# Optimization experiments

Hardware: AMD Instinct MI355X
Metric: run time of the kernel (lower is better)

The kernel has to match this reference:

```python
import jax, jax.numpy as jnp
import numpy as np

N_HEAD = 4
GROUPS = 32
EPS = 1e-5


def _group_norm(x, w, b):
    B, C, H, W = x.shape
    g = x.reshape(B, GROUPS, C // GROUPS, H, W)
    mu = g.mean(axis=(2, 3, 4), keepdims=True)
    var = ((g - mu) ** 2).mean(axis=(2, 3, 4), keepdims=True)
    g = (g - mu) * jax.lax.rsqrt(var + EPS)
    return g.reshape(B, C, H, W) * w[None, :, None, None] + b[None, :, None, None]


def _l2norm(x):
    # F.normalize(x, dim=-1): x / max(||x||_2, 1e-12)
    n = jnp.sqrt(jnp.sum(x * x, axis=-1, keepdims=True))
    return x / jnp.maximum(n, 1e-12)


def _masked_softmax(attn, kk):
    # topk indices -> scatter 1s -> masked softmax (faithful to torch scatter_ path)
    idx = jax.lax.top_k(attn, kk)[1]                      # [B,H,c,kk]
    mask = jax.nn.one_hot(idx, attn.shape[-1], dtype=attn.dtype).sum(-2)  # [B,H,c,c]
    return jax.nn.softmax(jnp.where(mask > 0, attn, -jnp.inf), axis=-1)


def setup_inputs() -> dict:
    key = jax.random.key(0)
    ks = jax.random.split(key, 8)
    B, C, H, W = 4, 256, 128, 128
    x = jax.random.normal(ks[0], (B, C, H, W), jnp.float32)
    gn_w = 1.0 + 0.02 * jax.random.normal(ks[1], (C,), jnp.float32)
    gn_b = 0.02 * jax.random.normal(ks[2], (C,), jnp.float32)
    w_qkv = jax.random.normal(ks[3], (3 * C, C), jnp.float32) / np.sqrt(C).astype(np.float32)
    w_dw = jax.random.normal(ks[4], (3 * C, 1, 3, 3), jnp.float32) / 3.0
    w_out = jax.random.normal(ks[5], (C, C), jnp.float32) / np.sqrt(C).astype(np.float32)
    b_out = 0.01 * jax.random.normal(ks[6], (C,), jnp.float32)
    temperature = jnp.ones((N_HEAD, 1, 1), jnp.float32)
    attn_w = jnp.full((4,), 0.2, jnp.float32)  # attn1..attn4 combine weights
    return dict(x=x, gn_w=gn_w, gn_b=gn_b, w_qkv=w_qkv, w_dw=w_dw,
                w_out=w_out, b_out=b_out, temperature=temperature, attn_w=attn_w)


def reference(x, gn_w, gn_b, w_qkv, w_dw, w_out, b_out, temperature, attn_w):
    B, C, H, W = x.shape
    c = C // N_HEAD
    xn = _group_norm(x, gn_w, gn_b)
    # 1x1 conv (no bias)
    qkv = jnp.einsum('oi,bihw->bohw', w_qkv, xn)
    # 3x3 depthwise conv, padding=1, groups=3C, no bias
    qkv = jax.lax.conv_general_dilated(
        qkv, w_dw, window_strides=(1, 1), padding=((1, 1), (1, 1)),
        feature_group_count=3 * C,
        dimension_numbers=('NCHW', 'OIHW', 'NCHW'))
    q, k, v = jnp.split(qkv, 3, axis=1)
    # b (head c) h w -> b head c (h w)
    q = q.reshape(B, N_HEAD, c, H * W)
    k = k.reshape(B, N_HEAD, c, H * W)
    v = v.reshape(B, N_HEAD, c, H * W)
    q = _l2norm(q)
    k = _l2norm(k)
    # FFT cross-correlation attention (fftshift over ALL axes, as torch default)
    q_fft = jnp.fft.fftshift(jnp.fft.rfft2(q))   # [B,H,c,HW//2+1] complex
    k_fft = jnp.fft.fftshift(jnp.fft.rfft2(k))
    attn = jnp.einsum('bhcf,bhdf->bhcd', q_fft, k_fft) * temperature  # complex [B,H,c,c]
    attn = jnp.fft.irfft2(jnp.fft.ifftshift(attn), s=(c, c))          # real [B,H,c,c]
    ks_list = [c // 2, (c * 2) // 3, (c * 3) // 4, (c * 4) // 5]
    out = None
    for i, kk in enumerate(ks_list):
        a = _masked_softmax(attn, kk)
        o = jnp.einsum('bhcd,bhds->bhcs', a, v) * attn_w[i]
        out = o if out is None else out + o
    out = out.reshape(B, C, H, W)
    out = jnp.einsum('oi,bihw->bohw', w_out, out) + b_out[None, :, None, None]
    return out
```

## Files before the change

### kernel.cpp

```cpp
#include <hip/hip_runtime.h>
#include <math.h>

#define NC 256
#define CH3 768
#define HWSZ 16384

typedef __attribute__((ext_vector_type(8))) short short8;
typedef __attribute__((ext_vector_type(4))) float f32x4;
typedef __attribute__((ext_vector_type(4))) unsigned int u32x4;

static const size_t OFF_TW1   = 0;
static const size_t OFF_TW2   = 32768;
static const size_t OFF_HM    = 65536;
static const size_t OFF_SCALE = 65600;
static const size_t OFF_SHIFT = 66624;
static const size_t OFF_PACK  = 67648;
static const size_t OFF_AW    = 182336;
static const size_t OFF_GNP   = 444480;
static const size_t SHARED_END= 446528;

static const size_t R_QKV  = 0;
static const size_t R_SCR  = 12582912;
static const size_t R_H    = 25165824;
static const size_t R_PP   = 29360128;
static const size_t R_RP   = 30408704;
static const size_t R_ATTN = 31457280;
static const size_t R_ACOMB= 31473664;
static const size_t R_PS   = 31490048;
static const size_t R_RS   = 31506432;
static const size_t R_DWP  = 31522816;
static const size_t R_SSUM = 31532032;
static const size_t R_SALT = 31532800;
static const size_t R_SSQ  = 31533568;
static const size_t RSTRIDE= 31534336;

#define TDA_RH 0
#define TDA_RL 8192
#define TDA_IH 16384
#define TDA_IL 24576
#define ETA_RH 32768
#define ETA_RL 40960
#define ETA_IH 49152
#define ETA_IL 57344
#define STB_RH 65536
#define STB_RL 73728
#define STB_IH 81920
#define STB_IL 90112
#define STB_NIH 98304
#define STB_NIL 106496

#define AWQ_H 0
#define AWQ_L 98304
#define AWO_H 196608
#define AWO_L 229376

__device__ inline unsigned short b16rn(float x){
  unsigned u = __float_as_uint(x);
  return (unsigned short)((u + 0x7FFFu + ((u>>16)&1u)) >> 16);
}
__device__ inline unsigned int pk_hi(float x, float y){
  return (__float_as_uint(x)>>16) | (__float_as_uint(y) & 0xFFFF0000u);
}
__device__ inline unsigned int pk_lo(float x, float y){
  float xl = x - __uint_as_float(__float_as_uint(x) & 0xFFFF0000u);
  float yl = y - __uint_as_float(__float_as_uint(y) & 0xFFFF0000u);
  return (unsigned)b16rn(xl) | ((unsigned)b16rn(yl)<<16);
}
__device__ inline short8 ld8g(const unsigned int* p){ return *(const short8*)p; }

__global__ __launch_bounds__(256) void init_tables_k(float* __restrict__ ws){
  int idx = blockIdx.x*256 + threadIdx.x;
  float2* tw1 = (float2*)(ws + OFF_TW1);
  float2* tw2 = (float2*)(ws + OFF_TW2);
  unsigned int* pk = (unsigned int*)(ws + OFF_PACK);
  const double P2 = 6.283185307179586476925286766559005;
  int m = idx >> 7, k = idx & 127;
  double a2 = P2 * (double)(m*k) / 16384.0;
  tw1[idx] = make_float2((float)cos(a2), (float)(-sin(a2)));
  tw2[idx] = make_float2((float)cos(a2), (float)( sin(a2)));
  if (idx < 64){
    double acc = 0.0;
    for (int v = 1; v < 32; v++) acc += sin(P2 * (double)((v*idx) & 63) / 64.0);
    ws[OFF_HM + idx] = (float)(-acc / 32.0);
  }
  if (idx < 8192){
    int r = idx >> 6, kp = idx & 63;
    int k0 = 2*kp, k1 = 2*kp+1;
    double a0 = P2 * (double)((r*k0) & 127) / 128.0;
    double a1 = P2 * (double)((r*k1) & 127) / 128.0;
    float c0 = (float)cos(a0), c1 = (float)cos(a1);
    float s0 = (float)sin(a0), s1 = (float)sin(a1);
    pk[TDA_RH + idx] = pk_hi(c0, c1);  pk[TDA_RL + idx] = pk_lo(c0, c1);
    pk[TDA_IH + idx] = pk_hi(-s0,-s1); pk[TDA_IL + idx] = pk_lo(-s0,-s1);
    pk[ETA_RH + idx] = pk_hi(c0, c1);  pk[ETA_RL + idx] = pk_lo(c0, c1);
    pk[ETA_IH + idx] = pk_hi(s0, s1);  pk[ETA_IL + idx] = pk_lo(s0, s1);
    float sr0, si0, sr1, si1;
    {
      int d0 = (r - k0) & 127, d1 = (r - k1) & 127;
      if (d0 == 0){ sr0 = 64.f; si0 = 0.f; }
      else if ((d0 & 1) == 0){ sr0 = 0.f; si0 = 0.f; }
      else { double th = 3.1415926535897932384626 * (double)d0 / 128.0;
             sr0 = 1.f; si0 = (float)(cos(th)/sin(th)); }
      if (d1 == 0){ sr1 = 64.f; si1 = 0.f; }
      else if ((d1 & 1) == 0){ sr1 = 0.f; si1 = 0.f; }
      else { double th = 3.1415926535897932384626 * (double)d1 / 128.0;
             sr1 = 1.f; si1 = (float)(cos(th)/sin(th)); }
    }
    pk[STB_RH + idx]  = pk_hi(sr0, sr1);  pk[STB_RL + idx]  = pk_lo(sr0, sr1);
    pk[STB_IH + idx]  = pk_hi(si0, si1);  pk[STB_IL + idx]  = pk_lo(si0, si1);
    pk[STB_NIH + idx] = pk_hi(-si0,-si1); pk[STB_NIL + idx] = pk_lo(-si0,-si1);
  }
}

__global__ __launch_bounds__(256) void wpack_k(const float* __restrict__ wqkv, const float* __restrict__ wout,
                                               unsigned int* __restrict__ aw){
  int id = blockIdx.x*256 + threadIdx.x;
  int row = id >> 7, kp = id & 127;
  if (row < CH3){
    float v0 = wqkv[row*256 + 2*kp], v1 = wqkv[row*256 + 2*kp + 1];
    aw[AWQ_H + row*128 + kp] = pk_hi(v0, v1);
    aw[AWQ_L + row*128 + kp] = pk_lo(v0, v1);
  } else {
    int r2 = row - CH3;
    float v0 = wout[r2*256 + 2*kp], v1 = wout[r2*256 + 2*kp + 1];
    aw[AWO_H + r2*128 + kp] = pk_hi(v0, v1);
    aw[AWO_L + r2*128 + kp] = pk_lo(v0, v1);
  }
}

__global__ __launch_bounds__(256) void gn_part_k(const float* __restrict__ x, float2* __restrict__ part){
  int id = blockIdx.x;
  const float4* p = (const float4*)(x + (size_t)id*HWSZ);
  int tid = threadIdx.x;
  float s = 0.f, sq = 0.f;
  #pragma unroll
  for (int i = 0; i < 16; i++){
    float4 v = p[tid + i*256];
    s  += v.x+v.y+v.z+v.w;
    sq += v.x*v.x+v.y*v.y+v.z*v.z+v.w*v.w;
  }
  __shared__ float r1[256], r2[256];
  r1[tid]=s; r2[tid]=sq; __syncthreads();
  for (int off=128; off; off>>=1){
    if (tid<off){ r1[tid]+=r1[tid+off]; r2[tid]+=r2[tid+off]; }
    __syncthreads();
  }
  if (tid==0) part[id] = make_float2(r1[0], r2[0]);
}
__global__ __launch_bounds__(128) void gn_fin_k(const float2* __restrict__ part, const float* __restrict__ gw,
                                                const float* __restrict__ gb, float* __restrict__ scale,
                                                float* __restrict__ shift){
  int bg = threadIdx.x;
  int b = bg >> 5, g = bg & 31;
  float s = 0.f, sq = 0.f;
  #pragma unroll
  for (int i = 0; i < 8; i++){
    float2 v = part[b*NC + g*8 + i];
    s += v.x; sq += v.y;
  }
  const float n = 8.0f*HWSZ;
  float mu = s/n, var = sq/n - mu*mu;
  float rs = rsqrtf(var + 1e-5f);
  for (int i = 0; i < 8; i++){
    int ch = g*8 + i;
    float sc = rs * gw[ch];
    scale[b*NC + ch] = sc;
    shift[b*NC + ch] = gb[ch] - mu*sc;
  }
}

__global__ __launch_bounds__(256) void packx_k(const float* __restrict__ xbase, const float* __restrict__ scale,
                                               const float* __restrict__ shift, float* __restrict__ R0,
                                               size_t rstride){
  int bz = blockIdx.z;
  const float* xb = xbase + (size_t)bz*NC*HWSZ;
  const float* sc = scale + bz*NC;
  const float* sh = shift + bz*NC;
  unsigned int* BqH = (unsigned int*)(R0 + (size_t)bz*rstride + R_H);
  unsigned int* BqL = BqH + 2097152;
  int kb = blockIdx.y;
  int n = blockIdx.x*256 + threadIdx.x;
  float v[8];
  #pragma unroll
  for (int c = 0; c < 8; c++){
    int ch = kb*8 + c;
    v[c] = xb[(size_t)ch*HWSZ + n]*sc[ch] + sh[ch];
  }
  u32x4 h, l;
  #pragma unroll
  for (int q = 0; q < 4; q++){
    h[q] = pk_hi(v[2*q], v[2*q+1]);
    l[q] = pk_lo(v[2*q], v[2*q+1]);
  }
  *(u32x4*)&BqH[((size_t)kb*HWSZ + n)*4] = h;
  *(u32x4*)&BqL[((size_t)kb*HWSZ + n)*4] = l;
}

__global__ __launch_bounds__(256) void gemm_pk(const unsigned int* __restrict__ Ah, const unsigned int* __restrict__ Al,
                                               const unsigned int* __restrict__ Bh0, const unsigned int* __restrict__ Bl0,
                                               const float* __restrict__ bias, float* __restrict__ C0,
                                               size_t bstride, size_t cstride){
  const unsigned int* Bh = Bh0 + (size_t)blockIdx.z*bstride;
  const unsigned int* Bl = Bl0 + (size_t)blockIdx.z*bstride;
  float* C = C0 + (size_t)blockIdx.z*cstride;
  int tid = threadIdx.x;
  int lane = tid & 63, wid = tid >> 6;
  int m0 = blockIdx.y*128, n0 = blockIdx.x*128;
  int wr = (wid>>1)*64, wc = (wid&1)*64;
  int lr = lane & 15, lk = lane >> 4;
  f32x4 acc[4][4] = {};
  size_t aoff[4], boff[4];
  #pragma unroll
  for (int i=0;i<4;i++) aoff[i] = (size_t)(m0 + wr + i*16 + lr)*128 + lk*4;
  #pragma unroll
  for (int j=0;j<4;j++) boff[j] = ((size_t)lk*HWSZ + n0 + wc + j*16 + lr)*4;
  short8 aH[2][4], aL[2][4], bH[2][4], bL[2][4];
  #pragma unroll
  for (int i=0;i<4;i++){ aH[0][i] = ld8g(Ah + aoff[i]); aL[0][i] = ld8g(Al + aoff[i]); }
  #pragma unroll
  for (int j=0;j<4;j++){ bH[0][j] = ld8g(Bh + boff[j]); bL[0][j] = ld8g(Bl + boff[j]); }
  #pragma unroll
  for (int kt = 0; kt < 8; kt++){
    int cur = kt & 1, nxt = cur ^ 1;
    if (kt < 7){
      size_t da = (size_t)(kt+1)*16;
      size_t db = (size_t)(kt+1)*4*HWSZ*4;
      #pragma unroll
      for (int i=0;i<4;i++){ aH[nxt][i] = ld8g(Ah + aoff[i] + da); aL[nxt][i] = ld8g(Al + aoff[i] + da); }
      #pragma unroll
      for (int j=0;j<4;j++){ bH[nxt][j] = ld8g(Bh + boff[j] + db); bL[nxt][j] = ld8g(Bl + boff[j] + db); }
    }
    #pragma unroll
    for (int i=0;i<4;i++)
      #pragma unroll
      for (int j=0;j<4;j++){
        acc[i][j] = __builtin_amdgcn_mfma_f32_16x16x32_bf16(aH[cur][i], bH[cur][j], acc[i][j], 0,0,0);
        acc[i][j] = __builtin_amdgcn_mfma_f32_16x16x32_bf16(aH[cur][i], bL[cur][j], acc[i][j], 0,0,0);
        acc[i][j] = __builtin_amdgcn_mfma_f32_16x16x32_bf16(aL[cur][i], bH[cur][j], acc[i][j], 0,0,0);
      }
  }
  #pragma unroll
  for (int i=0;i<4;i++){
    #pragma unroll
    for (int e=0;e<4;e++){
      int row = m0 + wr + i*16 + lk*4 + e;
      float bb = bias ? bias[row] : 0.0f;
      #pragma unroll
      for (int j=0;j<4;j++)
        C[(size_t)row*HWSZ + n0 + wc + j*16 + lr] = acc[i][j][e] + bb;
    }
  }
}

__global__ __launch_bounds__(256) void dwconv_tiled_k(float* __restrict__ R0, size_t rstride,
                                                      const float* __restrict__ wdw){
  float* Rb = R0 + (size_t)blockIdx.y*rstride;
  int blk = blockIdx.x;
  int ch = blk >> 2, sl = blk & 3;
  int h0 = sl*32;
  const float* in = Rb + R_SCR + (size_t)ch*HWSZ;
  float* outp = Rb + R_QKV + (size_t)ch*HWSZ;
  float* part = Rb + R_DWP;
  float w[9];
  #pragma unroll
  for (int i=0;i<9;i++) w[i] = wdw[ch*9+i];
  __shared__ float tile[34][132];
  __shared__ float r0[256], r1[256], r2[256];
  int tid = threadIdx.x;
  #pragma unroll
  for (int i = 0; i < 5; i++){
    int id = tid + i*256;
    if (id < 1088){
      int r = id >> 5, c4 = id & 31;
      int gh = h0 - 1 + r;
      float4 v = (gh >= 0 && gh < 128) ? *(const float4*)&in[gh*128 + c4*4]
                                       : make_float4(0.f,0.f,0.f,0.f);
      *(float4*)&tile[r][c4*4] = v;
    }
  }
  __syncthreads();
  float s=0.f, sa=0.f, sq=0.f;
  #pragma unroll
  for (int it=0; it<4; it++){
    int idx = it*256 + tid;
    int lh = idx >> 5;
    int xq = idx & 31;
    int xb4 = xq*4;
    float o[4];
    #pragma unroll
    for (int e=0;e<4;e++){
      int xw = xb4 + e;
      float acc = 0.f;
      #pragma unroll
      for (int ky=0; ky<3; ky++){
        const float* tr = &tile[lh+1+ky-1][xw];
        if (xw > 0)   acc += tr[-1]*w[ky*3+0];
                      acc += tr[ 0]*w[ky*3+1];
        if (xw < 127) acc += tr[ 1]*w[ky*3+2];
      }
      o[e] = acc;
      s += acc; sq += acc*acc;
      sa += (e & 1) ? -acc : acc;
    }
    *(float4*)&outp[(h0+lh)*128 + xb4] = make_float4(o[0],o[1],o[2],o[3]);
  }
  r0[tid]=s; r1[tid]=sa; r2[tid]=sq; __syncthreads();
  for (int off=128; off; off>>=1){
    if (tid<off){ r0[tid]+=r0[tid+off]; r1[tid]+=r1[tid+off]; r2[tid]+=r2[tid+off]; }
    __syncthreads();
  }
  if (tid==0){ part[blk]=r0[0]; part[3072+blk]=r1[0]; part[6144+blk]=r2[0]; }
}

__global__ __launch_bounds__(256) void fft1_mfma_k(const float* __restrict__ ws, float* __restrict__ R0,
                                                   size_t rstride){
  float* Rb = R0 + (size_t)blockIdx.y*rstride;
  const float* Kb = Rb + R_QKV + (size_t)256*HWSZ;
  float2* Tc = (float2*)(Rb + R_SCR);
  const unsigned int* PK = (const unsigned int*)(ws + OFF_PACK);
  const float2* tw1 = (const float2*)(ws + OFF_TW1);
  __shared__ unsigned int Bth[128][20], Btl[128][20];
  int tid = threadIdx.x;
  int lane = tid & 63, wid = tid >> 6;
  int wr = (wid>>1)*64, wc = (wid&1)*64;
  int lr = lane & 15, lk = lane >> 4;
  int row = blockIdx.x;
  const float* src = Kb + (size_t)row*HWSZ;
  f32x4 aR[4][4] = {}, aI[4][4] = {};
  int bc = tid & 127, grp = tid >> 7;
  for (int kt = 0; kt < 4; kt++){
    #pragma unroll
    for (int p=0;p<8;p++){
      int kp = grp*8 + p;
      int a = kt*32 + 2*kp;
      float v0 = src[a*128 + bc], v1 = src[(a+1)*128 + bc];
      Bth[bc][kp] = pk_hi(v0, v1);
      Btl[bc][kp] = pk_lo(v0, v1);
    }
    __syncthreads();
    short8 bh[4], bl[4];
    #pragma unroll
    for (int j=0;j<4;j++){
      bh[j] = *(const short8*)&Bth[wc + j*16 + lr][lk*4];
      bl[j] = *(const short8*)&Btl[wc + j*16 + lr][lk*4];
    }
    #pragma unroll
    for (int i=0;i<4;i++){
      int off = (wr + i*16 + lr)*64 + kt*16 + lk*4;
      short8 ahR = ld8g(PK + TDA_RH + off), alR = ld8g(PK + TDA_RL + off);
      short8 ahI = ld8g(PK + TDA_IH + off), alI = ld8g(PK + TDA_IL + off);
      #pragma unroll
      for (int j=0;j<4;j++){
        aR[i][j] = __builtin_amdgcn_mfma_f32_16x16x32_bf16(ahR, bh[j], aR[i][j], 0,0,0);
        aR[i][j] = __builtin_amdgcn_mfma_f32_16x16x32_bf16(ahR, bl[j], aR[i][j], 0,0,0);
        aR[i][j] = __builtin_amdgcn_mfma_f32_16x16x32_bf16(alR, bh[j], aR[i][j], 0,0,0);
        aI[i][j] = __builtin_amdgcn_mfma_f32_16x16x32_bf16(ahI, bh[j], aI[i][j], 0,0,0);
        aI[i][j] = __builtin_amdgcn_mfma_f32_16x16x32_bf16(ahI, bl[j], aI[i][j], 0,0,0);
        aI[i][j] = __builtin_amdgcn_mfma_f32_16x16x32_bf16(alI, bh[j], aI[i][j], 0,0,0);
      }
    }
    __syncthreads();
  }
  #pragma unroll
  for (int i=0;i<4;i++)
    #pragma unroll
    for (int e=0;e<4;e++){
      int m = wr + i*16 + lk*4 + e;
      #pragma unroll
      for (int j=0;j<4;j++){
        int col = wc + j*16 + lr;
        float2 t = tw1[m*128 + col];
        float r = aR[i][j][e], im = aI[i][j][e];
        Tc[(size_t)m*32768 + row*128 + col] = make_float2(r*t.x - im*t.y, r*t.y + im*t.x);
      }
    }
}

__global__ __launch_bounds__(256) void fft2_mfma_k(const float* __restrict__ ws, float* __restrict__ R0,
                                                   size_t rstride){
  float* Rb = R0 + (size_t)blockIdx.y*rstride;
  float2* TU = (float2*)(Rb + R_SCR);
  const unsigned int* PK = (const unsigned int*)(ws + OFF_PACK);
  const float2* tw2 = (const float2*)(ws + OFF_TW2);
  __shared__ unsigned int ARh[128][20], ARl[128][20], AIh[128][20], AIl[128][20];
  int tid = threadIdx.x;
  int lane = tid & 63, wid = tid >> 6;
  int wr = (wid>>1)*64, wc = (wid&1)*64;
  int lr = lane & 15, lk = lane >> 4;
  int m0 = blockIdx.x*128;
  f32x4 aR[4][4] = {}, aI[4][4] = {};
  const float* Tf = (const float*)TU;
  for (int kt = 0; kt < 4; kt++){
    #pragma unroll
    for (int s=0;s<8;s++){
      int id = tid + s*256;
      int r = id >> 4, kp = id & 15;
      int k = kt*32 + 2*kp;
      float4 v = *(const float4*)&Tf[((size_t)(m0+r)*128 + k)*2];
      ARh[r][kp] = pk_hi(v.x, v.z); ARl[r][kp] = pk_lo(v.x, v.z);
      AIh[r][kp] = pk_hi(v.y, v.w); AIl[r][kp] = pk_lo(v.y, v.w);
    }
    __syncthreads();
    short8 ahR[4], alR[4], ahI[4], alI[4];
    #pragma unroll
    for (int i=0;i<4;i++){
      int ar = wr + i*16 + lr;
      ahR[i] = *(const short8*)&ARh[ar][lk*4];
      alR[i] = *(const short8*)&ARl[ar][lk*4];
      ahI[i] = *(const short8*)&AIh[ar][lk*4];
      alI[i] = *(const short8*)&AIl[ar][lk*4];
    }
    #pragma unroll
    for (int j=0;j<4;j++){
      int boff = (wc + j*16 + lr)*64 + kt*16 + lk*4;
      short8 bhR = ld8g(PK + STB_RH + boff), blR = ld8g(PK + STB_RL + boff);
      short8 bhI = ld8g(PK + STB_IH + boff), blI = ld8g(PK + STB_IL + boff);
      short8 bhN = ld8g(PK + STB_NIH + boff), blN = ld8g(PK + STB_NIL + boff);
      #pragma unroll
      for (int i=0;i<4;i++){
        aR[i][j] = __builtin_amdgcn_mfma_f32_16x16x32_bf16(ahR[i], bhR, aR[i][j], 0,0,0);
        aR[i][j] = __builtin_amdgcn_mfma_f32_16x16x32_bf16(ahR[i], blR, aR[i][j], 0,0,0);
        aR[i][j] = __builtin_amdgcn_mfma_f32_16x16x32_bf16(alR[i], bhR, aR[i][j], 0,0,0);
        aR[i][j] = __builtin_amdgcn_mfma_f32_16x16x32_bf16(ahI[i], bhN, aR[i][j], 0,0,0);
        aR[i][j] = __builtin_amdgcn_mfma_f32_16x16x32_bf16(ahI[i], blN, aR[i][j], 0,0,0);
        aR[i][j] = __builtin_amdgcn_mfma_f32_16x16x32_bf16(alI[i], bhN, aR[i][j], 0,0,0);
        aI[i][j] = __builtin_amdgcn_mfma_f32_16x16x32_bf16(ahR[i], bhI, aI[i][j], 0,0,0);
        aI[i][j] = __builtin_amdgcn_mfma_f32_16x16x32_bf16(ahR[i], blI, aI[i][j], 0,0,0);
        aI[i][j] = __builtin_amdgcn_mfma_f32_16x16x32_bf16(alR[i], bhI, aI[i][j], 0,0,0);
        aI[i][j] = __builtin_amdgcn_mfma_f32_16x16x32_bf16(ahI[i], bhR, aI[i][j], 0,0,0);
        aI[i][j] = __builtin_amdgcn_mfma_f32_16x16x32_bf16(ahI[i], blR, aI[i][j], 0,0,0);
        aI[i][j] = __builtin_amdgcn_mfma_f32_16x16x32_bf16(alI[i], bhR, aI[i][j], 0,0,0);
      }
    }
    __syncthreads();
  }
  #pragma unroll
  for (int i=0;i<4;i++)
    #pragma unroll
    for (int e=0;e<4;e++){
      int m = m0 + wr + i*16 + lk*4 + e;
      int f0 = m >> 8;
      #pragma unroll
      for (int j=0;j<4;j++){
        int col = wc + j*16 + lr;
        float2 t = tw2[f0*128 + col];
        float r = aR[i][j][e], im = aI[i][j][e];
        TU[(size_t)m*128 + col] = make_float2(r*t.x - im*t.y, r*t.y + im*t.x);
      }
    }
}

__global__ __launch_bounds__(256) void fft3_mfma_k(const float* __restrict__ ws, float* __restrict__ R0,
                                                   size_t rstride){
  float* Rb = R0 + (size_t)blockIdx.y*rstride;
  const float2* U = (const float2*)(Rb + R_SCR);
  float* Hb = Rb + R_H;
  const unsigned int* PK = (const unsigned int*)(ws + OFF_PACK);
  __shared__ unsigned int BRh[128][20], BRl[128][20], BIh[128][20], BIl[128][20];
  int tid = threadIdx.x;
  int lane = tid & 63, wid = tid >> 6;
  int wr = (wid>>1)*64, wc = (wid&1)*64;
  int lr = lane & 15, lk = lane >> 4;
  int brow = blockIdx.x;
  f32x4 ac[4][4] = {};
  int bc = tid & 127, grp = tid >> 7;
  for (int kt = 0; kt < 4; kt++){
    #pragma unroll
    for (int p=0;p<8;p++){
      int kp = grp*8 + p;
      int k = kt*32 + 2*kp;
      float2 v0 = U[((size_t)k*256 + brow)*128 + bc];
      float2 v1 = U[((size_t)(k+1)*256 + brow)*128 + bc];
      BRh[bc][kp] = pk_hi(v0.x, v1.x); BRl[bc][kp] = pk_lo(v0.x, v1.x);
      BIh[bc][kp] = pk_hi(v0.y, v1.y); BIl[bc][kp] = pk_lo(v0.y, v1.y);
    }
    __syncthreads();
    short8 ahR[4], alR[4], ahI[4], alI[4];
    #pragma unroll
    for (int i=0;i<4;i++){
      int off = (wr + i*16 + lr)*64 + kt*16 + lk*4;
      ahR[i] = ld8g(PK + ETA_RH + off); alR[i] = ld8g(PK + ETA_RL + off);
      ahI[i] = ld8g(PK + ETA_IH + off); alI[i] = ld8g(PK + ETA_IL + off);
    }
    #pragma unroll
    for (int j=0;j<4;j++){
      int col = wc + j*16 + lr;
      short8 bhR = *(const short8*)&BRh[col][lk*4];
      short8 blR = *(const short8*)&BRl[col][lk*4];
      short8 bhI = *(const short8*)&BIh[col][lk*4];
      short8 blI = *(const short8*)&BIl[col][lk*4];
      #pragma unroll
      for (int i=0;i<4;i++){
        ac[i][j] = __builtin_amdgcn_mfma_f32_16x16x32_bf16(ahR[i], bhI, ac[i][j], 0,0,0);
        ac[i][j] = __builtin_amdgcn_mfma_f32_16x16x32_bf16(ahR[i], blI, ac[i][j], 0,0,0);
        ac[i][j] = __builtin_amdgcn_mfma_f32_16x16x32_bf16(alR[i], bhI, ac[i][j], 0,0,0);
        ac[i][j] = __builtin_amdgcn_mfma_f32_16x16x32_bf16(ahI[i], bhR, ac[i][j], 0,0,0);
        ac[i][j] = __builtin_amdgcn_mfma_f32_16x16x32_bf16(ahI[i], blR, ac[i][j], 0,0,0);
        ac[i][j] = __builtin_amdgcn_mfma_f32_16x16x32_bf16(alI[i], bhR, ac[i][j], 0,0,0);
      }
    }
    __syncthreads();
  }
  #pragma unroll
  for (int i=0;i<4;i++)
    #pragma unroll
    for (int e=0;e<4;e++){
      int m = wr + i*16 + lk*4 + e;
      #pragma unroll
      for (int j=0;j<4;j++)
        Hb[(size_t)m*32768 + brow*128 + wc + j*16 + lr] = ac[i][j][e];
    }
}

__global__ __launch_bounds__(256) void pri_k(float* __restrict__ R0, size_t rstride){
  float* Rb = R0 + (size_t)blockIdx.z*rstride;
  const float* qkvdw = Rb + R_QKV;
  const float* Hb = Rb + R_H;
  float* Pp = Rb + R_PP;
  float* Rp = Rb + R_RP;
  int sp = blockIdx.x, head = blockIdx.y;
  const float* Qb = qkvdw + (size_t)(head*64)*HWSZ;
  const float* Kb = qkvdw + (size_t)(256 + head*64)*HWSZ;
  int rowg0 = head*64;
  __shared__ float As[16][65], B1[16][65], B2[16][65];
  int tid=threadIdx.x, tx=tid&15, ty=tid>>4;
  float aP[4][4]={}, aR[4][4]={};
  for (int kc=0;kc<16;kc++){
    int s0 = sp*256 + kc*16;
    #pragma unroll
    for (int i=0;i<4;i++){ int id=tid+i*256; int kk=id&15, m=id>>4;
      As[kk][m] = Qb[(size_t)m*HWSZ + s0+kk]; }
    #pragma unroll
    for (int i=0;i<4;i++){ int id=tid+i*256; int kk=id&15, dd=id>>4;
      int t = (16384 - (s0+kk)) & 16383;
      B1[kk][dd] = Kb[(size_t)dd*HWSZ + t];
      int u = t>>7, r = t&127;
      B2[kk][dd] = Hb[(size_t)u*32768 + (size_t)(rowg0+dd)*128 + r]; }
    __syncthreads();
    #pragma unroll
    for (int k=0;k<16;k++){
      float a[4], b1[4], b2[4];
      #pragma unroll
      for (int i=0;i<4;i++) a[i]=As[k][ty*4+i];
      #pragma unroll
      for (int j=0;j<4;j++){ b1[j]=B1[k][tx*4+j]; b2[j]=B2[k][tx*4+j]; }
      #pragma unroll
      for (int i=0;i<4;i++)
        #pragma unroll
        for (int j=0;j<4;j++){ aP[i][j]+=a[i]*b1[j]; aR[i][j]+=a[i]*b2[j]; }
    }
    __syncthreads();
  }
  size_t base = ((size_t)(sp*4+head))<<12;
  #pragma unroll
  for (int i=0;i<4;i++)
    #pragma unroll
    for (int j=0;j<4;j++){
      size_t o = base + (size_t)(ty*4+i)*64 + tx*4+j;
      Pp[o]=aP[i][j]; Rp[o]=aR[i][j];
    }
}

__global__ __launch_bounds__(256) void red_k(float* __restrict__ R0, size_t rstride){
  float* Rb = R0 + (size_t)blockIdx.y*rstride;
  const float* Pp = Rb + R_PP;
  const float* Rp = Rb + R_RP;
  float* Ps = Rb + R_PS;
  float* Rs = Rb + R_RS;
  int tid = threadIdx.x;
  #pragma unroll
  for (int rep=0; rep<2; rep++){
    int g = blockIdx.x*512 + rep*256 + tid;
    int head = g >> 12, loc = g & 4095;
    float p = 0.f, ri = 0.f;
    for (int sp=0; sp<64; sp++){
      size_t o = ((size_t)(sp*4+head)<<12) + loc;
      p += Pp[o]; ri += Rp[o];
    }
    Ps[g] = p; Rs[g] = ri;
  }
  if (blockIdx.x == 0){
    const float* part = Rb + R_DWP;
    for (int ch = tid; ch < CH3; ch += 256){
      float s=0.f, sa=0.f, sq=0.f;
      #pragma unroll
      for (int sl=0; sl<4; sl++){
        s  += part[ch*4+sl];
        sa += part[3072+ch*4+sl];
        sq += part[6144+ch*4+sl];
      }
      Rb[R_SSUM+ch]=s; Rb[R_SALT+ch]=sa; Rb[R_SSQ+ch]=sq;
    }
  }
}

__global__ __launch_bounds__(256) void attn_build_k(const float* __restrict__ ws, float* __restrict__ R0,
                                                    size_t rstride, const float* __restrict__ temperature){
  float* Rb = R0 + (size_t)blockIdx.y*rstride;
  const float* Ps   = Rb + R_PS;
  const float* Rs   = Rb + R_RS;
  const float* ssum = Rb + R_SSUM;
  const float* salt = Rb + R_SALT;
  const float* ssq  = Rb + R_SSQ;
  float* attn = Rb + R_ATTN;
  const float* hmg  = ws + OFF_HM;
  __shared__ float Rn[64][65], Ril[64][65], hm[64];
  int head = blockIdx.x;
  int tid = threadIdx.x;
  if (tid < 64) hm[tid] = hmg[tid];
  for (int t=0;t<16;t++){
    int idx = tid + t*256; int c = idx>>6, d = idx&63;
    float P = Ps[head*4096 + idx], Ri = Rs[head*4096 + idx];
    int qch = head*64 + c;
    int kch = 256 + head*64 + d;
    float qs=ssum[qch], qa=salt[qch], qn=fmaxf(sqrtf(ssq[qch]), 1e-12f);
    float ks=ssum[kch], ka=salt[kch], kn=fmaxf(sqrtf(ssq[kch]), 1e-12f);
    float Rr = 0.5f*(16384.0f*P + qs*ks + qa*ka);
    float sc = 1.0f/(qn*kn);
    Rn[c][d]  = Rr*sc;
    Ril[c][d] = Ri*sc;
  }
  __syncthreads();
  float tmp2 = temperature[(head+2)&3];
  for (int t=0;t<16;t++){
    int idx = tid + t*256; int c = idx>>6, e = idx&63;
    float s = Rn[c][e];
    #pragma unroll 8
    for (int d=0; d<64; d++) s += Ril[c][d]*hm[(e-d)&63];
    attn[((size_t)head<<12) + (size_t)(c*64+e)] = s*tmp2;
  }
}

__global__ __launch_bounds__(64) void topk_k(float* __restrict__ R0, size_t rstride,
                                             const float* __restrict__ attn_w){
  float* Rb = R0 + (size_t)blockIdx.y*rstride;
  const float* attn = Rb + R_ATTN;
  float* Acomb = Rb + R_ACOMB;
  int blk = blockIdx.x;
  int tid = threadIdx.x;
  __shared__ float row[64];
  float v = attn[(size_t)blk*64 + tid];
  row[tid] = v;
  __syncthreads();
  int rank = 0; float vmax = -1e30f;
  for (int l=0;l<64;l++){
    float w = row[l];
    if (w > v || (w == v && l < tid)) rank++;
    vmax = fmaxf(vmax, w);
  }
  float e = expf(v - vmax);
  const int kks[4] = {32,42,48,51};
  float denom[4];
  #pragma unroll
  for (int i=0;i<4;i++){
    float x = (rank < kks[i]) ? e : 0.0f;
    #pragma unroll
    for (int off=32; off; off>>=1) x += __shfl_xor(x, off);
    denom[i] = x;
  }
  float wgt = 0.f;
  #pragma unroll
  for (int i=0;i<4;i++) if (rank < kks[i]) wgt += attn_w[i] / denom[i];
  Acomb[(size_t)blk*64 + tid] = e * wgt;
}

__global__ __launch_bounds__(256) void av_k(float* __restrict__ R0, size_t rstride){
  float* Rb = R0 + (size_t)blockIdx.z*rstride;
  const float* Acomb = Rb + R_ACOMB;
  unsigned int* BqH = (unsigned int*)(Rb + R_H);
  unsigned int* BqL = BqH + 2097152;
  int head = blockIdx.y;
  int n0 = blockIdx.x*64;
  const float* Vb = Rb + R_QKV + (size_t)(512 + head*64)*HWSZ;
  __shared__ float As[64][65], Bs[16][65];
  int tid=threadIdx.x, tx=tid&15, ty=tid>>4;
  for (int t=0;t<16;t++){ int idx=tid+t*256; As[idx>>6][idx&63] = Acomb[((size_t)head<<12)+idx]; }
  __syncthreads();
  float acc[4][4]={};
  for (int k0=0;k0<64;k0+=16){
    #pragma unroll
    for (int i=0;i<4;i++){ int id=tid+i*256; int nn=id&63, k=id>>6;
      Bs[k][nn] = Vb[(size_t)(k0+k)*HWSZ + n0+nn]; }
    __syncthreads();
    #pragma unroll
    for (int k=0;k<16;k++){
      float a[4], bv[4];
      #pragma unroll
      for (int i=0;i<4;i++) a[i]=As[ty*4+i][k0+k];
      #pragma unroll
      for (int j=0;j<4;j++) bv[j]=Bs[k][tx*4+j];
      #pragma unroll
      for (int i=0;i<4;i++)
        #pragma unroll
        for (int j=0;j<4;j++) acc[i][j] += a[i]*bv[j];
    }
    __syncthreads();
  }
  int kpa = head*32 + ty*2;
  int kba = kpa >> 2, qa = kpa & 3;
  int kpb = kpa + 1;
  int kbb = kpb >> 2, qb = kpb & 3;
  #pragma unroll
  for (int j=0;j<4;j++){
    int n = n0 + tx*4 + j;
    BqH[((size_t)kba*HWSZ + n)*4 + qa] = pk_hi(acc[0][j], acc[1][j]);
    BqL[((size_t)kba*HWSZ + n)*4 + qa] = pk_lo(acc[0][j], acc[1][j]);
    BqH[((size_t)kbb*HWSZ + n)*4 + qb] = pk_hi(acc[2][j], acc[3][j]);
    BqL[((size_t)kbb*HWSZ + n)*4 + qb] = pk_lo(acc[2][j], acc[3][j]);
  }
}

extern "C" void kernel_launch(void* const* d_in, const int* in_sizes, int n_in,
                              void* d_out, int out_size, void* d_ws, size_t ws_size,
                              hipStream_t stream) {
  const float* x     = (const float*)d_in[0];
  const float* gn_w  = (const float*)d_in[1];
  const float* gn_b  = (const float*)d_in[2];
  const float* w_qkv = (const float*)d_in[3];
  const float* w_dw  = (const float*)d_in[4];
  const float* w_out = (const float*)d_in[5];
  const float* b_out = (const float*)d_in[6];
  const float* temperature = (const float*)d_in[7];
  const float* attn_w = (const float*)d_in[8];
  float* out = (float*)d_out;
  float* ws  = (float*)d_ws;
  unsigned int* AW = (unsigned int*)(ws + OFF_AW);
  float* R0 = ws + SHARED_END;
  const size_t CHW = (size_t)NC*HWSZ;

  size_t need2 = (SHARED_END + 2*RSTRIDE)*sizeof(float);
  size_t need4 = (SHARED_END + 4*RSTRIDE)*sizeof(float);
  int zb = (ws_size >= need4) ? 4 : (ws_size >= need2) ? 2 : 1;

  init_tables_k<<<64,256,0,stream>>>(ws);
  wpack_k<<<512,256,0,stream>>>(w_qkv, w_out, AW);
  gn_part_k<<<1024,256,0,stream>>>(x, (float2*)(ws+OFF_GNP));
  gn_fin_k<<<1,128,0,stream>>>((const float2*)(ws+OFF_GNP), gn_w, gn_b,
                               ws+OFF_SCALE, ws+OFF_SHIFT);

  for (int b0 = 0; b0 < 4; b0 += zb){
    packx_k<<<dim3(64,32,zb),256,0,stream>>>(x + (size_t)b0*CHW, ws+OFF_SCALE+b0*NC,
                                             ws+OFF_SHIFT+b0*NC, R0, RSTRIDE);
    gemm_pk<<<dim3(128,6,zb),256,0,stream>>>(AW+AWQ_H, AW+AWQ_L,
                                             (unsigned int*)(R0+R_H), (unsigned int*)(R0+R_H)+2097152,
                                             nullptr, R0+R_SCR, RSTRIDE, RSTRIDE);
    dwconv_tiled_k<<<dim3(3072,zb),256,0,stream>>>(R0, RSTRIDE, w_dw);
    fft1_mfma_k<<<dim3(256,zb),256,0,stream>>>(ws, R0, RSTRIDE);
    fft2_mfma_k<<<dim3(256,zb),256,0,stream>>>(ws, R0, RSTRIDE);
    fft3_mfma_k<<<dim3(256,zb),256,0,stream>>>(ws, R0, RSTRIDE);
    pri_k<<<dim3(64,4,zb),256,0,stream>>>(R0, RSTRIDE);
    red_k<<<dim3(32,zb),256,0,stream>>>(R0, RSTRIDE);
    attn_build_k<<<dim3(4,zb),256,0,stream>>>(ws, R0, RSTRIDE, temperature);
    topk_k<<<dim3(256,zb),64,0,stream>>>(R0, RSTRIDE, attn_w);
    av_k<<<dim3(256,4,zb),256,0,stream>>>(R0, RSTRIDE);
    gemm_pk<<<dim3(128,2,zb),256,0,stream>>>(AW+AWO_H, AW+AWO_L,
                                             (unsigned int*)(R0+R_H), (unsigned int*)(R0+R_H)+2097152,
                                             b_out, out + (size_t)b0*CHW, RSTRIDE, CHW);
  }
}
```

Before: 859.1 us.

## Move pri correlation to split-bf16 MFMA and pre-reverse fft3 output layout

Rewrites the pri kernel from scalar FP32 FMA tiles to split-bf16 (hi/lo) MFMA, with operands packed into LDS. fft3 now writes its output already index-reversed and laid out per row, so pri reads it contiguously instead of through a strided gather. The projection GEMM also moves from double to triple register buffering of global loads, which raises register pressure. The split-bf16 trick drops the lo*lo term, so the correlation loses a little precision compared with full FP32.

Measured after the change: 828.4 us. -3.6%, faster.

```diff
diff --git a/kernel.cpp b/kernel.cpp
--- a/kernel.cpp
+++ b/kernel.cpp
@@ -214,22 +214,19 @@
   for (int i=0;i<4;i++) aoff[i] = (size_t)(m0 + wr + i*16 + lr)*128 + lk*4;
   #pragma unroll
   for (int j=0;j<4;j++) boff[j] = ((size_t)lk*HWSZ + n0 + wc + j*16 + lr)*4;
-  short8 aH[2][4], aL[2][4], bH[2][4], bL[2][4];
-  #pragma unroll
-  for (int i=0;i<4;i++){ aH[0][i] = ld8g(Ah + aoff[i]); aL[0][i] = ld8g(Al + aoff[i]); }
-  #pragma unroll
-  for (int j=0;j<4;j++){ bH[0][j] = ld8g(Bh + boff[j]); bL[0][j] = ld8g(Bl + boff[j]); }
+  short8 aH[3][4], aL[3][4], bH[3][4], bL[3][4];
+#define LOADT(B,T) { \
+    size_t da = (size_t)(T)*16, db = (size_t)(T)*4*HWSZ*4; \
+    _Pragma("unroll") \
+    for (int i=0;i<4;i++){ aH[B][i] = ld8g(Ah + aoff[i] + da); aL[B][i] = ld8g(Al + aoff[i] + da); } \
+    _Pragma("unroll") \
+    for (int j=0;j<4;j++){ bH[B][j] = ld8g(Bh + boff[j] + db); bL[B][j] = ld8g(Bl + boff[j] + db); } \
+  }
+  LOADT(0,0); LOADT(1,1);
   #pragma unroll
   for (int kt = 0; kt < 8; kt++){
-    int cur = kt & 1, nxt = cur ^ 1;
-    if (kt < 7){
-      size_t da = (size_t)(kt+1)*16;
-      size_t db = (size_t)(kt+1)*4*HWSZ*4;
-      #pragma unroll
-      for (int i=0;i<4;i++){ aH[nxt][i] = ld8g(Ah + aoff[i] + da); aL[nxt][i] = ld8g(Al + aoff[i] + da); }
-      #pragma unroll
-      for (int j=0;j<4;j++){ bH[nxt][j] = ld8g(Bh + boff[j] + db); bL[nxt][j] = ld8g(Bl + boff[j] + db); }
-    }
+    int cur = kt % 3;
+    if (kt < 6){ int nb = (kt+2) % 3; LOADT(nb, kt+2); }
     #pragma unroll
     for (int i=0;i<4;i++)
       #pragma unroll
@@ -239,6 +236,7 @@
         acc[i][j] = __builtin_amdgcn_mfma_f32_16x16x32_bf16(aL[cur][i], bH[cur][j], acc[i][j], 0,0,0);
       }
   }
+#undef LOADT
   #pragma unroll
   for (int i=0;i<4;i++){
     #pragma unroll
@@ -293,7 +291,7 @@
       float acc = 0.f;
       #pragma unroll
       for (int ky=0; ky<3; ky++){
-        const float* tr = &tile[lh+1+ky-1][xw];
+        const float* tr = &tile[lh+ky][xw];
         if (xw > 0)   acc += tr[-1]*w[ky*3+0];
                       acc += tr[ 0]*w[ky*3+1];
         if (xw < 127) acc += tr[ 1]*w[ky*3+2];
@@ -454,7 +452,7 @@
                                                    size_t rstride){
   float* Rb = R0 + (size_t)blockIdx.y*rstride;
   const float2* U = (const float2*)(Rb + R_SCR);
-  float* Hb = Rb + R_H;
+  float* Hf = Rb + R_H;
   const unsigned int* PK = (const unsigned int*)(ws + OFF_PACK);
   __shared__ unsigned int BRh[128][20], BRl[128][20], BIh[128][20], BIl[128][20];
   int tid = threadIdx.x;
@@ -507,57 +505,82 @@
     for (int e=0;e<4;e++){
       int m = wr + i*16 + lk*4 + e;
       #pragma unroll
-      for (int j=0;j<4;j++)
-        Hb[(size_t)m*32768 + brow*128 + wc + j*16 + lr] = ac[i][j][e];
-    }
-}
-
-__global__ __launch_bounds__(256) void pri_k(float* __restrict__ R0, size_t rstride){
+      for (int j=0;j<4;j++){
+        int col = wc + j*16 + lr;
+        int s = (16384 - (m*128 + col)) & 16383;
+        Hf[(size_t)brow*16384 + s] = ac[i][j][e];
+      }
+    }
+}
+
+__global__ __launch_bounds__(256) void pri2_k(float* __restrict__ R0, size_t rstride){
   float* Rb = R0 + (size_t)blockIdx.z*rstride;
-  const float* qkvdw = Rb + R_QKV;
-  const float* Hb = Rb + R_H;
+  int sp = blockIdx.x, head = blockIdx.y;
+  const float* Qb = Rb + R_QKV + (size_t)(head*64)*HWSZ;
+  const float* Kb = Rb + R_QKV + (size_t)(256 + head*64)*HWSZ;
+  const float* Hf = Rb + R_H + (size_t)(head*64)*16384;
   float* Pp = Rb + R_PP;
   float* Rp = Rb + R_RP;
-  int sp = blockIdx.x, head = blockIdx.y;
-  const float* Qb = qkvdw + (size_t)(head*64)*HWSZ;
-  const float* Kb = qkvdw + (size_t)(256 + head*64)*HWSZ;
-  int rowg0 = head*64;
-  __shared__ float As[16][65], B1[16][65], B2[16][65];
-  int tid=threadIdx.x, tx=tid&15, ty=tid>>4;
-  float aP[4][4]={}, aR[4][4]={};
-  for (int kc=0;kc<16;kc++){
-    int s0 = sp*256 + kc*16;
-    #pragma unroll
-    for (int i=0;i<4;i++){ int id=tid+i*256; int kk=id&15, m=id>>4;
-      As[kk][m] = Qb[(size_t)m*HWSZ + s0+kk]; }
-    #pragma unroll
-    for (int i=0;i<4;i++){ int id=tid+i*256; int kk=id&15, dd=id>>4;
-      int t = (16384 - (s0+kk)) & 16383;
-      B1[kk][dd] = Kb[(size_t)dd*HWSZ + t];
-      int u = t>>7, r = t&127;
-      B2[kk][dd] = Hb[(size_t)u*32768 + (size_t)(rowg0+dd)*128 + r]; }
-    __syncthreads();
-    #pragma unroll
-    for (int k=0;k<16;k++){
-      float a[4], b1[4], b2[4];
-      #pragma unroll
-      for (int i=0;i<4;i++) a[i]=As[k][ty*4+i];
-      #pragma unroll
-      for (int j=0;j<4;j++){ b1[j]=B1[k][tx*4+j]; b2[j]=B2[k][tx*4+j]; }
-      #pragma unroll
-      for (int i=0;i<4;i++)
-        #pragma unroll
-        for (int j=0;j<4;j++){ aP[i][j]+=a[i]*b1[j]; aR[i][j]+=a[i]*b2[j]; }
-    }
-    __syncthreads();
-  }
-  size_t base = ((size_t)(sp*4+head))<<12;
-  #pragma unroll
-  for (int i=0;i<4;i++)
-    #pragma unroll
-    for (int j=0;j<4;j++){
-      size_t o = base + (size_t)(ty*4+i)*64 + tx*4+j;
-      Pp[o]=aP[i][j]; Rp[o]=aR[i][j];
+  __shared__ unsigned int Qh[64][17], Ql[64][17], K1h[64][17], K1l[64][17], K2h[64][17], K2l[64][17];
+  int tid = threadIdx.x, lane = tid & 63, wid = tid >> 6;
+  int wr = (wid>>1)*32, wc = (wid&1)*32;
+  int lr = lane & 15, lk = lane >> 4;
+  int sd = tid >> 2, sk0 = (tid & 3)*8;
+  f32x4 aP[2][2] = {}, aR[2][2] = {};
+  for (int kt = 0; kt < 8; kt++){
+    int s0 = sp*256 + kt*32;
+    float q[8], k1[8], k2[8];
+    #pragma unroll
+    for (int e=0;e<8;e++){
+      int s = s0 + sk0 + e;
+      q[e]  = Qb[(size_t)sd*HWSZ + s];
+      k1[e] = Kb[(size_t)sd*HWSZ + ((16384 - s) & 16383)];
+      k2[e] = Hf[(size_t)sd*16384 + s];
+    }
+    __syncthreads();
+    #pragma unroll
+    for (int p=0;p<4;p++){
+      int kp = (sk0>>1) + p;
+      Qh[sd][kp]  = pk_hi(q[2*p],  q[2*p+1]);  Ql[sd][kp]  = pk_lo(q[2*p],  q[2*p+1]);
+      K1h[sd][kp] = pk_hi(k1[2*p], k1[2*p+1]); K1l[sd][kp] = pk_lo(k1[2*p], k1[2*p+1]);
+      K2h[sd][kp] = pk_hi(k2[2*p], k2[2*p+1]); K2l[sd][kp] = pk_lo(k2[2*p], k2[2*p+1]);
+    }
+    __syncthreads();
+    short8 qh[2], ql[2], b1h[2], b1l[2], b2h[2], b2l[2];
+    #pragma unroll
+    for (int i=0;i<2;i++){
+      qh[i]  = *(const short8*)&Qh[wr + i*16 + lr][lk*4];
+      ql[i]  = *(const short8*)&Ql[wr + i*16 + lr][lk*4];
+      b1h[i] = *(const short8*)&K1h[wc + i*16 + lr][lk*4];
+      b1l[i] = *(const short8*)&K1l[wc + i*16 + lr][lk*4];
+      b2h[i] = *(const short8*)&K2h[wc + i*16 + lr][lk*4];
+      b2l[i] = *(const short8*)&K2l[wc + i*16 + lr][lk*4];
+    }
+    #pragma unroll
+    for (int i=0;i<2;i++)
+      #pragma unroll
+      for (int j=0;j<2;j++){
+        aP[i][j] = __builtin_amdgcn_mfma_f32_16x16x32_bf16(qh[i], b1h[j], aP[i][j], 0,0,0);
+        aP[i][j] = __builtin_amdgcn_mfma_f32_16x16x32_bf16(qh[i], b1l[j], aP[i][j], 0,0,0);
+        aP[i][j] = __builtin_amdgcn_mfma_f32_16x16x32_bf16(ql[i], b1h[j], aP[i][j], 0,0,0);
+        aR[i][j] = __builtin_amdgcn_mfma_f32_16x16x32_bf16(qh[i], b2h[j], aR[i][j], 0,0,0);
+        aR[i][j] = __builtin_amdgcn_mfma_f32_16x16x32_bf16(qh[i], b2l[j], aR[i][j], 0,0,0);
+        aR[i][j] = __builtin_amdgcn_mfma_f32_16x16x32_bf16(ql[i], b2h[j], aR[i][j], 0,0,0);
+      }
+  }
+  size_t base = ((size_t)(sp*4 + head)) << 12;
+  #pragma unroll
+  for (int i=0;i<2;i++)
+    #pragma unroll
+    for (int e=0;e<4;e++){
+      int row = wr + i*16 + lk*4 + e;
+      #pragma unroll
+      for (int j=0;j<2;j++){
+        int col = wc + j*16 + lr;
+        size_t o = base + (size_t)row*64 + col;
+        Pp[o] = aP[i][j][e];
+        Rp[o] = aR[i][j][e];
+      }
     }
 }
 
@@ -748,7 +771,7 @@
     fft1_mfma_k<<<dim3(256,zb),256,0,stream>>>(ws, R0, RSTRIDE);
     fft2_mfma_k<<<dim3(256,zb),256,0,stream>>>(ws, R0, RSTRIDE);
     fft3_mfma_k<<<dim3(256,zb),256,0,stream>>>(ws, R0, RSTRIDE);
-    pri_k<<<dim3(64,4,zb),256,0,stream>>>(R0, RSTRIDE);
+    pri2_k<<<dim3(64,4,zb),256,0,stream>>>(R0, RSTRIDE);
     red_k<<<dim3(32,zb),256,0,stream>>>(R0, RSTRIDE);
     attn_build_k<<<dim3(4,zb),256,0,stream>>>(ws, R0, RSTRIDE, temperature);
     topk_k<<<dim3(256,zb),64,0,stream>>>(R0, RSTRIDE, attn_w);
```

## Rewrite pri kernel with split-bf16 MFMA and pre-reversed bf16 operand layouts

Applied to the files above, without the earlier changes.

The fp32 scalar-FMA pri_k GEMM is replaced by pri3_k, which uses bf16x3-style split-precision MFMA instructions. The dwconv kernel now also emits Q as hi/lo bf16 pairs with the spatial index reversed, and K as hi/lo bf16 pairs. fft3 writes its output in a transposed hi/lo bf16 layout so pri3 can do contiguous vector loads instead of gathered strided loads. The aim is to remove the scalar FMA and gather cost, at the price of extra writes in dwconv and fft3 and reduced precision from the split-bf16 approximation.

Result: faster. 825.1 us (-4.0%).

```diff
diff --git a/kernel.cpp b/kernel.cpp
--- a/kernel.cpp
+++ b/kernel.cpp
@@ -33,6 +33,7 @@
 static const size_t R_SALT = 31532800;
 static const size_t R_SSQ  = 31533568;
 static const size_t RSTRIDE= 31534336;
+static const size_t HNOFF  = 8388608;
 
 #define TDA_RH 0
 #define TDA_RL 8192
@@ -259,7 +260,6 @@
   int ch = blk >> 2, sl = blk & 3;
   int h0 = sl*32;
   const float* in = Rb + R_SCR + (size_t)ch*HWSZ;
-  float* outp = Rb + R_QKV + (size_t)ch*HWSZ;
   float* part = Rb + R_DWP;
   float w[9];
   #pragma unroll
@@ -293,7 +293,7 @@
       float acc = 0.f;
       #pragma unroll
       for (int ky=0; ky<3; ky++){
-        const float* tr = &tile[lh+1+ky-1][xw];
+        const float* tr = &tile[lh+ky][xw];
         if (xw > 0)   acc += tr[-1]*w[ky*3+0];
                       acc += tr[ 0]*w[ky*3+1];
         if (xw < 127) acc += tr[ 1]*w[ky*3+2];
@@ -302,7 +302,32 @@
       s += acc; sq += acc*acc;
       sa += (e & 1) ? -acc : acc;
     }
-    *(float4*)&outp[(h0+lh)*128 + xb4] = make_float4(o[0],o[1],o[2],o[3]);
+    int sbase = (h0+lh)*128 + xb4;
+    if (ch < 256){
+      unsigned short* QHo = (unsigned short*)(Rb + R_QKV);
+      unsigned short* QLo = (unsigned short*)(Rb + R_QKV + 2097152);
+      size_t ro = (size_t)ch*HWSZ;
+      #pragma unroll
+      for (int e=0;e<4;e++){
+        int sf = (16384 - (sbase+e)) & 16383;
+        unsigned u = __float_as_uint(o[e]);
+        QHo[ro + sf] = (unsigned short)(u >> 16);
+        QLo[ro + sf] = b16rn(o[e] - __uint_as_float(u & 0xFFFF0000u));
+      }
+    } else if (ch < 512){
+      *(float4*)&(Rb + R_QKV + (size_t)ch*HWSZ)[sbase] = make_float4(o[0],o[1],o[2],o[3]);
+      unsigned short* KHo = (unsigned short*)(Rb + R_H);
+      unsigned short* KLo = (unsigned short*)(Rb + R_H + 2097152);
+      size_t ro = (size_t)(ch-256)*HWSZ;
+      #pragma unroll
+      for (int e=0;e<4;e++){
+        unsigned u = __float_as_uint(o[e]);
+        KHo[ro + sbase+e] = (unsigned short)(u >> 16);
+        KLo[ro + sbase+e] = b16rn(o[e] - __uint_as_float(u & 0xFFFF0000u));
+      }
+    } else {
+      *(float4*)&(Rb + R_QKV + (size_t)ch*HWSZ)[sbase] = make_float4(o[0],o[1],o[2],o[3]);
+    }
   }
   r0[tid]=s; r1[tid]=sa; r2[tid]=sq; __syncthreads();
   for (int off=128; off; off>>=1){
@@ -454,7 +479,8 @@
                                                    size_t rstride){
   float* Rb = R0 + (size_t)blockIdx.y*rstride;
   const float2* U = (const float2*)(Rb + R_SCR);
-  float* Hb = Rb + R_H;
+  unsigned short* HHo = (unsigned short*)(Rb + R_SCR + HNOFF);
+  unsigned short* HLo = (unsigned short*)(Rb + R_SCR + HNOFF + 2097152);
   const unsigned int* PK = (const unsigned int*)(ws + OFF_PACK);
   __shared__ unsigned int BRh[128][20], BRl[128][20], BIh[128][20], BIl[128][20];
   int tid = threadIdx.x;
@@ -507,57 +533,80 @@
     for (int e=0;e<4;e++){
       int m = wr + i*16 + lk*4 + e;
       #pragma unroll
-      for (int j=0;j<4;j++)
-        Hb[(size_t)m*32768 + brow*128 + wc + j*16 + lr] = ac[i][j][e];
-    }
-}
-
-__global__ __launch_bounds__(256) void pri_k(float* __restrict__ R0, size_t rstride){
+      for (int j=0;j<4;j++){
+        int col = wc + j*16 + lr;
+        float v = ac[i][j][e];
+        unsigned u = __float_as_uint(v);
+        size_t o = (size_t)brow*HWSZ + m*128 + col;
+        HHo[o] = (unsigned short)(u >> 16);
+        HLo[o] = b16rn(v - __uint_as_float(u & 0xFFFF0000u));
+      }
+    }
+}
+
+__global__ __launch_bounds__(256) void pri3_k(float* __restrict__ R0, size_t rstride){
   float* Rb = R0 + (size_t)blockIdx.z*rstride;
-  const float* qkvdw = Rb + R_QKV;
-  const float* Hb = Rb + R_H;
+  int sp = blockIdx.x, head = blockIdx.y;
+  const unsigned short* QH = (const unsigned short*)(Rb + R_QKV);
+  const unsigned short* QL = (const unsigned short*)(Rb + R_QKV + 2097152);
+  const unsigned short* KH = (const unsigned short*)(Rb + R_H);
+  const unsigned short* KL = (const unsigned short*)(Rb + R_H + 2097152);
+  const unsigned short* HH = (const unsigned short*)(Rb + R_SCR + HNOFF);
+  const unsigned short* HL = (const unsigned short*)(Rb + R_SCR + HNOFF + 2097152);
   float* Pp = Rb + R_PP;
   float* Rp = Rb + R_RP;
-  int sp = blockIdx.x, head = blockIdx.y;
-  const float* Qb = qkvdw + (size_t)(head*64)*HWSZ;
-  const float* Kb = qkvdw + (size_t)(256 + head*64)*HWSZ;
-  int rowg0 = head*64;
-  __shared__ float As[16][65], B1[16][65], B2[16][65];
-  int tid=threadIdx.x, tx=tid&15, ty=tid>>4;
-  float aP[4][4]={}, aR[4][4]={};
-  for (int kc=0;kc<16;kc++){
-    int s0 = sp*256 + kc*16;
-    #pragma unroll
-    for (int i=0;i<4;i++){ int id=tid+i*256; int kk=id&15, m=id>>4;
-      As[kk][m] = Qb[(size_t)m*HWSZ + s0+kk]; }
-    #pragma unroll
-    for (int i=0;i<4;i++){ int id=tid+i*256; int kk=id&15, dd=id>>4;
-      int t = (16384 - (s0+kk)) & 16383;
-      B1[kk][dd] = Kb[(size_t)dd*HWSZ + t];
-      int u = t>>7, r = t&127;
-      B2[kk][dd] = Hb[(size_t)u*32768 + (size_t)(rowg0+dd)*128 + r]; }
-    __syncthreads();
-    #pragma unroll
-    for (int k=0;k<16;k++){
-      float a[4], b1[4], b2[4];
-      #pragma unroll
-      for (int i=0;i<4;i++) a[i]=As[k][ty*4+i];
-      #pragma unroll
-      for (int j=0;j<4;j++){ b1[j]=B1[k][tx*4+j]; b2[j]=B2[k][tx*4+j]; }
-      #pragma unroll
-      for (int i=0;i<4;i++)
-        #pragma unroll
-        for (int j=0;j<4;j++){ aP[i][j]+=a[i]*b1[j]; aR[i][j]+=a[i]*b2[j]; }
-    }
-    __syncthreads();
-  }
-  size_t base = ((size_t)(sp*4+head))<<12;
-  #pragma unroll
-  for (int i=0;i<4;i++)
-    #pragma unroll
-    for (int j=0;j<4;j++){
-      size_t o = base + (size_t)(ty*4+i)*64 + tx*4+j;
-      Pp[o]=aP[i][j]; Rp[o]=aR[i][j];
+  int tid = threadIdx.x, lane = tid & 63, wid = tid >> 6;
+  int wr = (wid>>1)*32, wc = (wid&1)*32;
+  int lr = lane & 15, lk = lane >> 4;
+  size_t qoff[2], koff[2];
+  #pragma unroll
+  for (int i=0;i<2;i++) qoff[i] = (size_t)(head*64 + wr + i*16 + lr)*HWSZ + sp*256 + lk*8;
+  #pragma unroll
+  for (int j=0;j<2;j++) koff[j] = (size_t)(head*64 + wc + j*16 + lr)*HWSZ + sp*256 + lk*8;
+  f32x4 aP[2][2] = {}, aRi[2][2] = {};
+  short8 qh[2][2], ql[2][2], k1h[2][2], k1l[2][2], k2h[2][2], k2l[2][2];
+#define LDPRI(B,T) { int d = (T)*32; \
+    _Pragma("unroll") \
+    for (int i=0;i<2;i++){ \
+      qh[B][i] = *(const short8*)(QH + qoff[i] + d); \
+      ql[B][i] = *(const short8*)(QL + qoff[i] + d); } \
+    _Pragma("unroll") \
+    for (int j=0;j<2;j++){ \
+      k1h[B][j] = *(const short8*)(KH + koff[j] + d); \
+      k1l[B][j] = *(const short8*)(KL + koff[j] + d); \
+      k2h[B][j] = *(const short8*)(HH + koff[j] + d); \
+      k2l[B][j] = *(const short8*)(HL + koff[j] + d); } }
+  LDPRI(0,0);
+  #pragma unroll
+  for (int kt = 0; kt < 8; kt++){
+    int cur = kt & 1;
+    if (kt < 7) LDPRI(cur^1, kt+1);
+    #pragma unroll
+    for (int i=0;i<2;i++)
+      #pragma unroll
+      for (int j=0;j<2;j++){
+        aP[i][j]  = __builtin_amdgcn_mfma_f32_16x16x32_bf16(qh[cur][i], k1h[cur][j], aP[i][j], 0,0,0);
+        aP[i][j]  = __builtin_amdgcn_mfma_f32_16x16x32_bf16(qh[cur][i], k1l[cur][j], aP[i][j], 0,0,0);
+        aP[i][j]  = __builtin_amdgcn_mfma_f32_16x16x32_bf16(ql[cur][i], k1h[cur][j], aP[i][j], 0,0,0);
+        aRi[i][j] = __builtin_amdgcn_mfma_f32_16x16x32_bf16(qh[cur][i], k2h[cur][j], aRi[i][j], 0,0,0);
+        aRi[i][j] = __builtin_amdgcn_mfma_f32_16x16x32_bf16(qh[cur][i], k2l[cur][j], aRi[i][j], 0,0,0);
+        aRi[i][j] = __builtin_amdgcn_mfma_f32_16x16x32_bf16(ql[cur][i], k2h[cur][j], aRi[i][j], 0,0,0);
+      }
+  }
+#undef LDPRI
+  size_t obase = ((size_t)(sp*4 + head)) << 12;
+  #pragma unroll
+  for (int i=0;i<2;i++)
+    #pragma unroll
+    for (int e=0;e<4;e++){
+      int row = wr + i*16 + lk*4 + e;
+      #pragma unroll
+      for (int j=0;j<2;j++){
+        int col = wc + j*16 + lr;
+        size_t o = obase + (size_t)row*64 + col;
+        Pp[o] = aP[i][j][e];
+        Rp[o] = aRi[i][j][e];
+      }
     }
 }
 
@@ -748,7 +797,7 @@
     fft1_mfma_k<<<dim3(256,zb),256,0,stream>>>(ws, R0, RSTRIDE);
     fft2_mfma_k<<<dim3(256,zb),256,0,stream>>>(ws, R0, RSTRIDE);
     fft3_mfma_k<<<dim3(256,zb),256,0,stream>>>(ws, R0, RSTRIDE);
-    pri_k<<<dim3(64,4,zb),256,0,stream>>>(R0, RSTRIDE);
+    pri3_k<<<dim3(64,4,zb),256,0,stream>>>(R0, RSTRIDE);
     red_k<<<dim3(32,zb),256,0,stream>>>(R0, RSTRIDE);
     attn_build_k<<<dim3(4,zb),256,0,stream>>>(ws, R0, RSTRIDE, temperature);
     topk_k<<<dim3(256,zb),64,0,stream>>>(R0, RSTRIDE, attn_w);
```
